# Kernel optimization log

Measured on AMD Instinct MI355X. Metric: run time of the kernel, lower is better.

Reference implementation:

```python
import jax, jax.numpy as jnp
import numpy as np

B, LQ, LC, LN, D, H = 4, 1024, 1024, 1024, 1024, 16
HD = D // H
LS_INIT = 1e-4
RES_MAX = 10.0
EPS = 1e-5


def layernorm(x, g, b):
    mu = jnp.mean(x, axis=-1, keepdims=True)
    var = jnp.var(x, axis=-1, keepdims=True)
    return (x - mu) * jax.lax.rsqrt(var + EPS) * g + b


def setup_inputs() -> dict:
    key = jax.random.key(0)
    ks = jax.random.split(key, 12)
    s = 0.02
    return {
        "tight_tokens": jax.random.normal(ks[0], (B, LQ, D), jnp.float32),
        "context_tokens": jax.random.normal(ks[1], (B, LC, D), jnp.float32),
        "neighborhood_tokens": jax.random.normal(ks[2], (B, LN, D), jnp.float32),
        "ln_q_g": jnp.ones((D,), jnp.float32), "ln_q_b": jnp.zeros((D,), jnp.float32),
        "ln_kv_g": jnp.ones((D,), jnp.float32), "ln_kv_b": jnp.zeros((D,), jnp.float32),
        "in_proj_w": jax.random.normal(ks[3], (3 * D, D), jnp.float32) * s,
        "in_proj_b": jnp.zeros((3 * D,), jnp.float32),
        "out_proj_w": jax.random.normal(ks[4], (D, D), jnp.float32) * s,
        "out_proj_b": jnp.zeros((D,), jnp.float32),
        "cross_gamma": jnp.full((D,), LS_INIT, jnp.float32),
        "ln_f_g": jnp.ones((D,), jnp.float32), "ln_f_b": jnp.zeros((D,), jnp.float32),
        "w1": jax.random.normal(ks[5], (4 * D, D), jnp.float32) * s,
        "b1": jnp.zeros((4 * D,), jnp.float32),
        "w2": jax.random.normal(ks[6], (D, 4 * D), jnp.float32) * s,
        "b2": jnp.zeros((D,), jnp.float32),
        "ffn_gamma": jnp.full((D,), LS_INIT, jnp.float32),
    }


def reference(tight_tokens, context_tokens, neighborhood_tokens,
              ln_q_g, ln_q_b, ln_kv_g, ln_kv_b,
              in_proj_w, in_proj_b, out_proj_w, out_proj_b, cross_gamma,
              ln_f_g, ln_f_b, w1, b1, w2, b2, ffn_gamma):
    kv = jnp.concatenate([context_tokens, neighborhood_tokens], axis=1)  # [B, LKV, D]
    q_in = layernorm(tight_tokens, ln_q_g, ln_q_b)
    kv_in = layernorm(kv, ln_kv_g, ln_kv_b)

    wq, wk, wv = jnp.split(in_proj_w, 3, axis=0)
    bq, bk, bv = jnp.split(in_proj_b, 3, axis=0)
    q = (q_in @ wq.T + bq).reshape(B, LQ, H, HD)
    k = (kv_in @ wk.T + bk).reshape(B, -1, H, HD)
    v = (kv_in @ wv.T + bv).reshape(B, -1, H, HD)

    scores = jnp.einsum('bqhd,bkhd->bhqk', q, k) / jnp.sqrt(jnp.float32(HD))
    attn = jax.nn.softmax(scores, axis=-1)  # [B, H, LQ, LKV]
    ctx = jnp.einsum('bhqk,bkhd->bqhd', attn, v).reshape(B, LQ, D)
    attn_out = ctx @ out_proj_w.T + out_proj_b

    cg = jnp.clip(cross_gamma, -RES_MAX, RES_MAX)
    x = tight_tokens + attn_out * cg

    h = layernorm(x, ln_f_g, ln_f_b)
    h = jax.nn.gelu(h @ w1.T + b1, approximate=False) @ w2.T + b2
    fg = jnp.clip(ffn_gamma, -RES_MAX, RES_MAX)
    x = x + h * fg

    return x, attn.mean(axis=1)
```

## Files before the change

### kernel.cpp

```cpp
#include <hip/hip_runtime.h>
#include <math.h>

typedef unsigned short u16;
typedef __attribute__((ext_vector_type(8))) short bf16x8;
typedef __attribute__((ext_vector_type(4))) float f32x4;

#define MFMA16(a,b,c) __builtin_amdgcn_mfma_f32_16x16x32_bf16(a,b,c,0,0,0)

__device__ __forceinline__ u16 f2bf(float f){
  union { float f; unsigned int u; } x; x.f = f;
  unsigned int r = x.u + 0x7fffu + ((x.u >> 16) & 1u);
  return (u16)(r >> 16);
}

__device__ __forceinline__ void gload16(const void* g, void* lds){
  __builtin_amdgcn_global_load_lds(
    (const __attribute__((address_space(1))) unsigned int*)g,
    (__attribute__((address_space(3))) unsigned int*)lds, 16, 0, 0);
}

__global__ __launch_bounds__(256) void cvt_weights(
    const float* __restrict__ wqkv, const float* __restrict__ wo,
    const float* __restrict__ w1, const float* __restrict__ w2,
    u16* __restrict__ o0, u16* __restrict__ o1,
    u16* __restrict__ o2, u16* __restrict__ o3)
{
  int idx = blockIdx.x * 256 + threadIdx.x;
  const float* src; u16* dst;
  if (idx < 786432)                    { src = wqkv; dst = o0; }
  else if ((idx -= 786432) < 262144)   { src = wo;   dst = o1; }
  else if ((idx -= 262144) < 1048576)  { src = w1;   dst = o2; }
  else { idx -= 1048576;                 src = w2;   dst = o3; }
  float4 v = ((const float4*)src)[idx];
  short4 o;
  o.x = (short)f2bf(v.x); o.y = (short)f2bf(v.y);
  o.z = (short)f2bf(v.z); o.w = (short)f2bf(v.w);
  ((short4*)dst)[idx] = o;
}

template<int MODE>
__global__ __launch_bounds__(256) void ln_kernel(
    const float* __restrict__ s0, const float* __restrict__ s1,
    const float* __restrict__ g, const float* __restrict__ be,
    u16* __restrict__ out)
{
  int row = blockIdx.x, t = threadIdx.x;
  const float* src;
  if (MODE == 1) {
    int b = row >> 11, p = row & 2047;
    src = (p < 1024) ? s0 + ((long)(b*1024 + p))*1024
                     : s1 + ((long)(b*1024 + p - 1024))*1024;
  } else {
    src = s0 + (long)row * 1024;
  }
  float4 v = ((const float4*)src)[t];
  float s  = v.x + v.y + v.z + v.w;
  float ss = v.x*v.x + v.y*v.y + v.z*v.z + v.w*v.w;
  #pragma unroll
  for (int m = 1; m < 64; m <<= 1) { s += __shfl_xor(s, m); ss += __shfl_xor(ss, m); }
  __shared__ float red[8];
  int l = t & 63, w = t >> 6;
  if (l == 0) { red[w*2] = s; red[w*2+1] = ss; }
  __syncthreads();
  s  = red[0] + red[2] + red[4] + red[6];
  ss = red[1] + red[3] + red[5] + red[7];
  float mean = s * (1.0f/1024.0f);
  float var  = ss * (1.0f/1024.0f) - mean*mean;
  float rstd = rsqrtf(var + 1e-5f);
  float4 gv = ((const float4*)g)[t];
  float4 bv = ((const float4*)be)[t];
  short4 o;
  o.x = (short)f2bf((v.x-mean)*rstd*gv.x + bv.x);
  o.y = (short)f2bf((v.y-mean)*rstd*gv.y + bv.y);
  o.z = (short)f2bf((v.z-mean)*rstd*gv.z + bv.z);
  o.w = (short)f2bf((v.w-mean)*rstd*gv.w + bv.w);
  *(short4*)(out + (long)row*1024 + t*4) = o;
}

template<int EPI, int BM>
__global__ __launch_bounds__(256,2) void gemm_bt(
    const u16* __restrict__ A, const u16* __restrict__ Bt,
    int M, int N, int K,
    const float* __restrict__ bias,
    const float* __restrict__ gamma,
    const float* __restrict__ resid,
    float* __restrict__ outf,
    u16* __restrict__ outb0, u16* __restrict__ outb1)
{
  constexpr int MI = BM / 32;
  __shared__ __align__(16) u16 at[2][BM*64];
  __shared__ __align__(16) u16 bt[2][128*64];
  int nwg = gridDim.x;
  int bidx = (blockIdx.x & 7) * (nwg >> 3) + (blockIdx.x >> 3);
  int nb = N >> 7;
  int tm = bidx / nb, tn = bidx % nb;
  int m0 = tm * BM, n0 = tn << 7;
  int t = threadIdx.x, l = t & 63, w = t >> 6;
  int wr = (w >> 1) * (BM/2), wc = (w & 1) * 64;
  int fr = l & 15, fq = l >> 4;
  f32x4 acc[MI][4] = {};
  int rr = t >> 3;
  int cb = (t & 7) << 4;
  const char* Ab = (const char*)A;
  const char* Bp = (const char*)Bt;
  long ld = (long)K * 2;

#define G_STAGE(s, kt) do {                                                        \
    _Pragma("unroll")                                                              \
    for (int c = 0; c < MI; c++) {                                                 \
      int row = c*32 + rr;                                                         \
      gload16(Ab + (long)(m0 + row)*ld + (long)(kt)*2 + (cb ^ ((row & 7) << 4)),   \
              (char*)at[s] + c*4096 + w*1024);                                     \
    }                                                                              \
    _Pragma("unroll")                                                              \
    for (int c = 0; c < 4; c++) {                                                  \
      int row = c*32 + rr;                                                         \
      gload16(Bp + (long)(n0 + row)*ld + (long)(kt)*2 + (cb ^ ((row & 7) << 4)),   \
              (char*)bt[s] + c*4096 + w*1024);                                     \
    }                                                                              \
  } while (0)

  G_STAGE(0, 0);
  __syncthreads();
  int cur = 0;
  for (int kt = 0; kt < K; kt += 64) {
    if (kt + 64 < K) G_STAGE(cur ^ 1, kt + 64);
    #pragma unroll
    for (int ka = 0; ka < 2; ka++) {
      bf16x8 af[MI], bfv[4];
      #pragma unroll
      for (int i = 0; i < MI; i++) {
        int ra = wr + i*16 + fr;
        af[i] = *(const bf16x8*)((const char*)at[cur] + ra*128 + ((ka*64 + fq*16) ^ ((ra & 7) << 4)));
      }
      #pragma unroll
      for (int j = 0; j < 4; j++) {
        int rb = wc + j*16 + fr;
        bfv[j] = *(const bf16x8*)((const char*)bt[cur] + rb*128 + ((ka*64 + fq*16) ^ ((rb & 7) << 4)));
      }
      #pragma unroll
      for (int i = 0; i < MI; i++)
        #pragma unroll
        for (int j = 0; j < 4; j++)
          acc[i][j] = MFMA16(af[i], bfv[j], acc[i][j]);
    }
    __syncthreads();
    cur ^= 1;
  }
#undef G_STAGE
  #pragma unroll
  for (int i = 0; i < MI; i++) {
    #pragma unroll
    for (int j = 0; j < 4; j++) {
      #pragma unroll
      for (int r = 0; r < 4; r++) {
        int row = m0 + wr + i*16 + fq*4 + r;
        int col = n0 + wc + j*16 + fr;
        float v = acc[i][j][r];
        if constexpr (EPI == 0) {
          float qv = (v + bias[col]) * 0.18033688011112042f;
          int b = row >> 10, lq = row & 1023, h = col >> 6, hd = col & 63;
          outb0[(((long)(b*16 + h)) << 16) + (lq << 6) + hd] = f2bf(qv);
        } else if constexpr (EPI == 1) {
          float u = v + bias[col];
          int b = row >> 11, p = row & 2047;
          if (col < 1024) {
            int h = col >> 6, hd = col & 63;
            outb0[(((long)((b*16 + h)*2048 + p)) << 6) + hd] = f2bf(u);
          } else {
            int c2 = col - 1024, h = c2 >> 6, hd = c2 & 63;
            outb1[(((long)((b*16 + h)*64 + hd)) << 11) + p] = f2bf(u);
          }
        } else if constexpr (EPI == 2) {
          float gs = gamma[col]; gs = fminf(fmaxf(gs, -10.f), 10.f);
          long idx = (long)row*1024 + col;
          outf[idx] = resid[idx] + (v + bias[col]) * gs;
        } else if constexpr (EPI == 3) {
          float u = v + bias[col];
          float ge = 0.5f * u * (1.0f + erff(u * 0.70710678118654752f));
          outb0[(long)row*4096 + col] = f2bf(ge);
        } else {
          float gs = gamma[col]; gs = fminf(fmaxf(gs, -10.f), 10.f);
          long idx = (long)row*1024 + col;
          outf[idx] = resid[idx] + (v + bias[col]) * gs;
        }
      }
    }
  }
}

__global__ __launch_bounds__(256, 4) void flash_fwd(
    const u16* __restrict__ q, const u16* __restrict__ k,
    const u16* __restrict__ vt, u16* __restrict__ ctx,
    float* __restrict__ ilout)
{
  __shared__ __align__(16) u16 ks[2][64*64];
  __shared__ __align__(16) u16 vs[2][64*64];
  __shared__ __align__(16) char ps[4*2048];
  int nwg = gridDim.x;
  int bid = (blockIdx.x & 7) * (nwg >> 3) + (blockIdx.x >> 3);
  int qt = bid & 15, h = (bid >> 4) & 15, b = bid >> 8;
  int q0 = qt << 6;
  int t = threadIdx.x, l = t & 63, w = t >> 6;
  int fr = l & 15, fq = l >> 4;
  const char* qb = (const char*)(q  + (((long)(b*16 + h)) << 16));
  const char* kb = (const char*)(k  + (((long)(b*16 + h)) << 17));
  const char* vb = (const char*)(vt + (((long)(b*16 + h)) << 17));
  char* psw = ps + w*2048;
  int rr = t >> 3;
  int sc = (t & 7) << 4;

  #pragma unroll
  for (int c = 0; c < 2; c++) {
    int row = c*32 + rr;
    gload16(kb + (long)row*128 + (sc ^ ((row & 7) << 4)), (char*)ks[0] + c*4096 + w*1024);
    gload16(vb + (long)row*4096 + (sc ^ ((row & 7) << 4)), (char*)vs[0] + c*4096 + w*1024);
  }
  {
    int qr = l >> 3;
    #pragma unroll
    for (int c = 0; c < 2; c++) {
      int row = c*8 + qr;
      gload16(qb + (long)(q0 + w*16 + row)*128 + (sc ^ ((row & 7) << 4)), psw + c*1024);
    }
  }
  asm volatile("s_waitcnt vmcnt(0)" ::: "memory");
  bf16x8 qf0 = *(const bf16x8*)(psw + fr*128 + ((fq*16) ^ ((fr & 7) << 4)));
  bf16x8 qf1 = *(const bf16x8*)(psw + fr*128 + ((64 + fq*16) ^ ((fr & 7) << 4)));
  asm volatile("s_waitcnt lgkmcnt(0)" ::: "memory");
  __builtin_amdgcn_s_barrier();
  asm volatile("" ::: "memory");

  f32x4 cacc[4] = {};
  f32x4 lrun = {0.f, 0.f, 0.f, 0.f};
  int cur = 0;
  for (int kt = 0; kt < 2048; kt += 64) {
    int notlast = (kt + 64 < 2048);
    if (notlast) {
      #pragma unroll
      for (int c = 0; c < 2; c++) {
        int row = c*32 + rr;
        gload16(vb + (long)row*4096 + (long)(kt + 64)*2 + (sc ^ ((row & 7) << 4)),
                (char*)vs[cur ^ 1] + c*4096 + w*1024);
        gload16(kb + (long)(kt + 64 + row)*128 + (sc ^ ((row & 7) << 4)),
                (char*)ks[cur ^ 1] + c*4096 + w*1024);
      }
    }
    __builtin_amdgcn_sched_barrier(0);
    const char* ksb = (const char*)ks[cur];
    f32x4 sf[4];
    __builtin_amdgcn_s_setprio(1);
    #pragma unroll
    for (int cf = 0; cf < 4; cf++) {
      int row = cf*16 + fr;
      bf16x8 kf0 = *(const bf16x8*)(ksb + row*128 + ((fq*16) ^ ((row & 7) << 4)));
      bf16x8 kf1 = *(const bf16x8*)(ksb + row*128 + ((64 + fq*16) ^ ((row & 7) << 4)));
      f32x4 a = {};
      a = MFMA16(qf0, kf0, a);
      sf[cf] = MFMA16(qf1, kf1, a);
    }
    __builtin_amdgcn_s_setprio(0);
    #pragma unroll
    for (int cf = 0; cf < 4; cf++)
      #pragma unroll
      for (int r = 0; r < 4; r++) {
        float pv = exp2f(sf[cf][r]);
        lrun[r] += pv;
        union { float f; unsigned int u; } pu; pu.f = pv;
        int prow = fq*4 + r;
        *(u16*)(psw + prow*128 + (((cf*16 + fr) << 1) ^ ((prow & 7) << 4))) = (u16)(pu.u >> 16);
      }
    bf16x8 pa0 = *(const bf16x8*)(psw + fr*128 + ((fq*16) ^ ((fr & 7) << 4)));
    bf16x8 pa1 = *(const bf16x8*)(psw + fr*128 + ((64 + fq*16) ^ ((fr & 7) << 4)));
    __builtin_amdgcn_s_setprio(1);
    #pragma unroll
    for (int cfd = 0; cfd < 4; cfd++) {
      int hd = cfd*16 + fr;
      bf16x8 vf0 = *(const bf16x8*)((const char*)vs[cur] + hd*128 + ((fq*16) ^ ((hd & 7) << 4)));
      bf16x8 vf1 = *(const bf16x8*)((const char*)vs[cur] + hd*128 + ((64 + fq*16) ^ ((hd & 7) << 4)));
      cacc[cfd] = MFMA16(pa0, vf0, cacc[cfd]);
      cacc[cfd] = MFMA16(pa1, vf1, cacc[cfd]);
    }
    __builtin_amdgcn_s_setprio(0);
    if (notlast) {
      asm volatile("s_waitcnt vmcnt(0)" ::: "memory");
      __builtin_amdgcn_s_barrier();
      asm volatile("" ::: "memory");
    }
    cur ^= 1;
  }
  float il4[4];
  #pragma unroll
  for (int r = 0; r < 4; r++) {
    float s = lrun[r];
    #pragma unroll
    for (int msk = 1; msk < 16; msk <<= 1) s += __shfl_xor(s, msk, 16);
    il4[r] = 1.0f / s;
  }
  #pragma unroll
  for (int cf = 0; cf < 4; cf++)
    #pragma unroll
    for (int r = 0; r < 4; r++) {
      int row = q0 + w*16 + fq*4 + r;
      int col = h*64 + cf*16 + fr;
      ctx[(long)(b*1024 + row)*1024 + col] = f2bf(cacc[cf][r] * il4[r]);
    }
  if (fr == 0) {
    #pragma unroll
    for (int r = 0; r < 4; r++) {
      int row = q0 + w*16 + fq*4 + r;
      long idx = (((long)(b*16 + h)) << 10) + row;
      ilout[idx] = il4[r];
    }
  }
}

__global__ __launch_bounds__(256,2) void attn_mean(
    const u16* __restrict__ q, const u16* __restrict__ k,
    const float* __restrict__ il,
    float* __restrict__ out)
{
  __shared__ __align__(16) u16 qs[2][128*64];
  __shared__ __align__(16) u16 ks[2][128*64];
  __shared__ __align__(16) float ml[2][128];
  int nwg = gridDim.x;
  int bid = (blockIdx.x & 7) * (nwg >> 3) + (blockIdx.x >> 3);
  int kt = bid & 15, qt = (bid >> 4) & 7, b = bid >> 7;
  int q0 = qt << 7, k0 = kt << 7;
  int t = threadIdx.x, l = t & 63, w = t >> 6;
  int wr = (w >> 1) << 6, wc = (w & 1) << 6;
  int fr = l & 15, fq = l >> 4;
  int rr = t >> 3, cbb = (t & 7) << 4;
  const long bh = (long)b * 16;

#define AM_STAGE(hh, s) do {                                                        \
    const char* qb_ = (const char*)(q + ((bh + (hh)) << 16)) + (long)q0*128;        \
    const char* kb_ = (const char*)(k + ((bh + (hh)) << 17)) + (long)k0*128;        \
    _Pragma("unroll")                                                               \
    for (int c = 0; c < 4; c++) {                                                   \
      int row = c*32 + rr;                                                          \
      int sw = cbb ^ ((row & 7) << 4);                                              \
      gload16(qb_ + (long)row*128 + sw, (char*)qs[s] + c*4096 + w*1024);            \
      gload16(kb_ + (long)row*128 + sw, (char*)ks[s] + c*4096 + w*1024);            \
    }                                                                               \
    if (w == 0 && l < 32) {                                                         \
      gload16((const char*)(il + ((bh + (hh)) << 10) + q0) + l*16, (char*)ml[s]);   \
    }                                                                               \
  } while (0)

  AM_STAGE(0, 0);
  asm volatile("s_waitcnt vmcnt(0)" ::: "memory");
  __builtin_amdgcn_s_barrier();
  asm volatile("" ::: "memory");

  f32x4 macc[4][4] = {};
  for (int h = 0; h < 16; h++) {
    int cur = h & 1;
    if (h < 15) AM_STAGE(h + 1, cur ^ 1);
    const char* qsb = (const char*)qs[cur];
    const char* ksb = (const char*)ks[cur];
    const float* mlb = ml[cur];
    f32x4 ir4[4];
    #pragma unroll
    for (int i = 0; i < 4; i++)
      ir4[i] = *(const f32x4*)(mlb + wr + i*16 + fq*4);
    bf16x8 af[4][2], bf[4][2];
    #pragma unroll
    for (int i = 0; i < 4; i++) {
      int ra = wr + i*16 + fr;
      int rb = wc + i*16 + fr;
      af[i][0] = *(const bf16x8*)(qsb + ra*128 + ((fq*16) ^ ((ra & 7) << 4)));
      af[i][1] = *(const bf16x8*)(qsb + ra*128 + ((64 + fq*16) ^ ((ra & 7) << 4)));
      bf[i][0] = *(const bf16x8*)(ksb + rb*128 + ((fq*16) ^ ((rb & 7) << 4)));
      bf[i][1] = *(const bf16x8*)(ksb + rb*128 + ((64 + fq*16) ^ ((rb & 7) << 4)));
    }
    #pragma unroll
    for (int j = 0; j < 4; j++) {
      f32x4 sf[4];
      __builtin_amdgcn_s_setprio(1);
      #pragma unroll
      for (int i = 0; i < 4; i++) {
        f32x4 a = MFMA16(af[i][0], bf[j][0], {});
        sf[i] = MFMA16(af[i][1], bf[j][1], a);
      }
      __builtin_amdgcn_s_setprio(0);
      #pragma unroll
      for (int i = 0; i < 4; i++)
        #pragma unroll
        for (int r = 0; r < 4; r++)
          macc[i][j][r] += exp2f(sf[i][r]) * ir4[i][r];
    }
    asm volatile("s_waitcnt vmcnt(0)" ::: "memory");
    __builtin_amdgcn_s_barrier();
    asm volatile("" ::: "memory");
  }
#undef AM_STAGE
  #pragma unroll
  for (int i = 0; i < 4; i++)
    #pragma unroll
    for (int j = 0; j < 4; j++)
      #pragma unroll
      for (int r = 0; r < 4; r++) {
        int row = q0 + wr + i*16 + fq*4 + r;
        int col = k0 + wc + j*16 + fr;
        out[((long)(b*1024 + row) << 11) + col] = macc[i][j][r] * 0.0625f;
      }
}

extern "C" void kernel_launch(void* const* d_in, const int* in_sizes, int n_in,
                              void* d_out, int out_size, void* d_ws, size_t ws_size,
                              hipStream_t stream)
{
  (void)in_sizes; (void)n_in; (void)out_size; (void)ws_size;
  const float* tight = (const float*)d_in[0];
  const float* ctxt  = (const float*)d_in[1];
  const float* nbh   = (const float*)d_in[2];
  const float* lnqg  = (const float*)d_in[3];
  const float* lnqb  = (const float*)d_in[4];
  const float* lnkg  = (const float*)d_in[5];
  const float* lnkb  = (const float*)d_in[6];
  const float* wqkv  = (const float*)d_in[7];
  const float* bqkv  = (const float*)d_in[8];
  const float* wo    = (const float*)d_in[9];
  const float* bo    = (const float*)d_in[10];
  const float* cg    = (const float*)d_in[11];
  const float* lnfg  = (const float*)d_in[12];
  const float* lnfb  = (const float*)d_in[13];
  const float* w1    = (const float*)d_in[14];
  const float* b1    = (const float*)d_in[15];
  const float* w2    = (const float*)d_in[16];
  const float* b2    = (const float*)d_in[17];
  const float* fg    = (const float*)d_in[18];

  char* p = (char*)d_ws;
  u16* wqkv_bf = (u16*)p; p += 3072L*1024*2;
  u16* wo_bf   = (u16*)p; p += 1024L*1024*2;
  u16* w1_bf   = (u16*)p; p += 4096L*1024*2;
  u16* w2_bf   = (u16*)p; p += 1024L*4096*2;
  u16* qin_bf  = (u16*)p; p += 4096L*1024*2;
  u16* kvin_bf = (u16*)p; p += 8192L*1024*2;
  u16* q_bf    = (u16*)p; p += 4L*16*1024*64*2;
  u16* k_bf    = (u16*)p; p += 4L*16*2048*64*2;
  u16* vt_bf   = (u16*)p; p += 4L*16*64*2048*2;
  u16* ctx_bf  = (u16*)p; p += 4096L*1024*2;
  float* il_f  = (float*)p; p += 4L*16*1024*4;
  float* x_f   = (float*)p; p += 4096L*1024*4;
  u16* hln_bf  = (u16*)p; p += 4096L*1024*2;
  u16* gelu_bf = (u16*)p; p += 4096L*4096*2;

  float* x_out    = (float*)d_out;
  float* mean_out = x_out + 4194304;

  cvt_weights<<<12288, 256, 0, stream>>>(wqkv, wo, w1, w2, wqkv_bf, wo_bf, w1_bf, w2_bf);
  ln_kernel<0><<<4096, 256, 0, stream>>>(tight, nullptr, lnqg, lnqb, qin_bf);
  ln_kernel<1><<<8192, 256, 0, stream>>>(ctxt, nbh, lnkg, lnkb, kvin_bf);
  gemm_bt<0,64><<<512, 256, 0, stream>>>(qin_bf, wqkv_bf, 4096, 1024, 1024,
                                      bqkv, nullptr, nullptr, nullptr, q_bf, nullptr);
  gemm_bt<1,128><<<1024, 256, 0, stream>>>(kvin_bf, wqkv_bf + 1024L*1024, 8192, 2048, 1024,
                                       bqkv + 1024, nullptr, nullptr, nullptr, k_bf, vt_bf);
  flash_fwd<<<1024, 256, 0, stream>>>(q_bf, k_bf, vt_bf, ctx_bf, il_f);
  attn_mean<<<512, 256, 0, stream>>>(q_bf, k_bf, il_f, mean_out);
  gemm_bt<2,64><<<512, 256, 0, stream>>>(ctx_bf, wo_bf, 4096, 1024, 1024,
                                      bo, cg, tight, x_f, nullptr, nullptr);
  ln_kernel<0><<<4096, 256, 0, stream>>>(x_f, nullptr, lnfg, lnfb, hln_bf);
  gemm_bt<3,128><<<1024, 256, 0, stream>>>(hln_bf, w1_bf, 4096, 4096, 1024,
                                       b1, nullptr, nullptr, nullptr, gelu_bf, nullptr);
  gemm_bt<4,64><<<512, 256, 0, stream>>>(gelu_bf, w2_bf, 4096, 1024, 4096,
                                      b2, fg, x_f, x_out, nullptr, nullptr);
}
```

Baseline: 374.1 us.

## Double query rows per wave in flash attention to reuse K/V tiles

Each workgroup now handles 128 query rows instead of 64, with every wave computing two 16-row fragments that share the same K and V fragments loaded from LDS. This halves the number of K/V tile loads from global memory and the LDS fragment reads per MFMA, and the grid shrinks from 1024 to 512 workgroups. The cost is more registers and a larger P buffer in LDS, with occupancy lowered to 3 waves-per-SIMD bound, and fewer workgroups to spread across compute units.

New measurement: 371.7 us. About the same (-0.6%).

```diff
diff --git a/kernel.cpp b/kernel.cpp
--- a/kernel.cpp
+++ b/kernel.cpp
@@ -189,24 +189,24 @@
   }
 }
 
-__global__ __launch_bounds__(256, 4) void flash_fwd(
+__global__ __launch_bounds__(256, 3) void flash_fwd(
     const u16* __restrict__ q, const u16* __restrict__ k,
     const u16* __restrict__ vt, u16* __restrict__ ctx,
     float* __restrict__ ilout)
 {
   __shared__ __align__(16) u16 ks[2][64*64];
   __shared__ __align__(16) u16 vs[2][64*64];
-  __shared__ __align__(16) char ps[4*2048];
+  __shared__ __align__(16) char ps[4*4096];
   int nwg = gridDim.x;
   int bid = (blockIdx.x & 7) * (nwg >> 3) + (blockIdx.x >> 3);
-  int qt = bid & 15, h = (bid >> 4) & 15, b = bid >> 8;
-  int q0 = qt << 6;
+  int qt = bid & 7, h = (bid >> 3) & 15, b = bid >> 7;
+  int q0 = qt << 7;
   int t = threadIdx.x, l = t & 63, w = t >> 6;
   int fr = l & 15, fq = l >> 4;
   const char* qb = (const char*)(q  + (((long)(b*16 + h)) << 16));
   const char* kb = (const char*)(k  + (((long)(b*16 + h)) << 17));
   const char* vb = (const char*)(vt + (((long)(b*16 + h)) << 17));
-  char* psw = ps + w*2048;
+  char* psw = ps + w*4096;
   int rr = t >> 3;
   int sc = (t & 7) << 4;
 
@@ -219,20 +219,25 @@
   {
     int qr = l >> 3;
     #pragma unroll
-    for (int c = 0; c < 2; c++) {
+    for (int c = 0; c < 4; c++) {
       int row = c*8 + qr;
-      gload16(qb + (long)(q0 + w*16 + row)*128 + (sc ^ ((row & 7) << 4)), psw + c*1024);
+      gload16(qb + (long)(q0 + w*32 + row)*128 + (sc ^ ((row & 7) << 4)), psw + c*1024);
     }
   }
   asm volatile("s_waitcnt vmcnt(0)" ::: "memory");
-  bf16x8 qf0 = *(const bf16x8*)(psw + fr*128 + ((fq*16) ^ ((fr & 7) << 4)));
-  bf16x8 qf1 = *(const bf16x8*)(psw + fr*128 + ((64 + fq*16) ^ ((fr & 7) << 4)));
+  bf16x8 qf[2][2];
+  #pragma unroll
+  for (int rf = 0; rf < 2; rf++) {
+    int row = rf*16 + fr;
+    qf[rf][0] = *(const bf16x8*)(psw + row*128 + ((fq*16) ^ ((row & 7) << 4)));
+    qf[rf][1] = *(const bf16x8*)(psw + row*128 + ((64 + fq*16) ^ ((row & 7) << 4)));
+  }
   asm volatile("s_waitcnt lgkmcnt(0)" ::: "memory");
   __builtin_amdgcn_s_barrier();
   asm volatile("" ::: "memory");
 
-  f32x4 cacc[4] = {};
-  f32x4 lrun = {0.f, 0.f, 0.f, 0.f};
+  f32x4 cacc[2][4] = {};
+  f32x4 lrun[2] = {{0.f,0.f,0.f,0.f},{0.f,0.f,0.f,0.f}};
   int cur = 0;
   for (int kt = 0; kt < 2048; kt += 64) {
     int notlast = (kt + 64 < 2048);
@@ -248,38 +253,51 @@
     }
     __builtin_amdgcn_sched_barrier(0);
     const char* ksb = (const char*)ks[cur];
-    f32x4 sf[4];
+    f32x4 sf[2][4];
     __builtin_amdgcn_s_setprio(1);
     #pragma unroll
     for (int cf = 0; cf < 4; cf++) {
       int row = cf*16 + fr;
       bf16x8 kf0 = *(const bf16x8*)(ksb + row*128 + ((fq*16) ^ ((row & 7) << 4)));
       bf16x8 kf1 = *(const bf16x8*)(ksb + row*128 + ((64 + fq*16) ^ ((row & 7) << 4)));
-      f32x4 a = {};
-      a = MFMA16(qf0, kf0, a);
-      sf[cf] = MFMA16(qf1, kf1, a);
+      #pragma unroll
+      for (int rf = 0; rf < 2; rf++) {
+        f32x4 a = {};
+        a = MFMA16(qf[rf][0], kf0, a);
+        sf[rf][cf] = MFMA16(qf[rf][1], kf1, a);
+      }
     }
     __builtin_amdgcn_s_setprio(0);
     #pragma unroll
-    for (int cf = 0; cf < 4; cf++)
-      #pragma unroll
-      for (int r = 0; r < 4; r++) {
-        float pv = exp2f(sf[cf][r]);
-        lrun[r] += pv;
-        union { float f; unsigned int u; } pu; pu.f = pv;
-        int prow = fq*4 + r;
-        *(u16*)(psw + prow*128 + (((cf*16 + fr) << 1) ^ ((prow & 7) << 4))) = (u16)(pu.u >> 16);
-      }
-    bf16x8 pa0 = *(const bf16x8*)(psw + fr*128 + ((fq*16) ^ ((fr & 7) << 4)));
-    bf16x8 pa1 = *(const bf16x8*)(psw + fr*128 + ((64 + fq*16) ^ ((fr & 7) << 4)));
+    for (int rf = 0; rf < 2; rf++)
+      #pragma unroll
+      for (int cf = 0; cf < 4; cf++)
+        #pragma unroll
+        for (int r = 0; r < 4; r++) {
+          float pv = exp2f(sf[rf][cf][r]);
+          lrun[rf][r] += pv;
+          union { float f; unsigned int u; } pu; pu.f = pv;
+          int prow = rf*16 + fq*4 + r;
+          *(u16*)(psw + prow*128 + (((cf*16 + fr) << 1) ^ ((prow & 7) << 4))) = (u16)(pu.u >> 16);
+        }
+    bf16x8 pa[2][2];
+    #pragma unroll
+    for (int rf = 0; rf < 2; rf++) {
+      int row = rf*16 + fr;
+      pa[rf][0] = *(const bf16x8*)(psw + row*128 + ((fq*16) ^ ((row & 7) << 4)));
+      pa[rf][1] = *(const bf16x8*)(psw + row*128 + ((64 + fq*16) ^ ((row & 7) << 4)));
+    }
     __builtin_amdgcn_s_setprio(1);
     #pragma unroll
     for (int cfd = 0; cfd < 4; cfd++) {
       int hd = cfd*16 + fr;
       bf16x8 vf0 = *(const bf16x8*)((const char*)vs[cur] + hd*128 + ((fq*16) ^ ((hd & 7) << 4)));
       bf16x8 vf1 = *(const bf16x8*)((const char*)vs[cur] + hd*128 + ((64 + fq*16) ^ ((hd & 7) << 4)));
-      cacc[cfd] = MFMA16(pa0, vf0, cacc[cfd]);
-      cacc[cfd] = MFMA16(pa1, vf1, cacc[cfd]);
+      #pragma unroll
+      for (int rf = 0; rf < 2; rf++) {
+        cacc[rf][cfd] = MFMA16(pa[rf][0], vf0, cacc[rf][cfd]);
+        cacc[rf][cfd] = MFMA16(pa[rf][1], vf1, cacc[rf][cfd]);
+      }
     }
     __builtin_amdgcn_s_setprio(0);
     if (notlast) {
@@ -289,28 +307,31 @@
     }
     cur ^= 1;
   }
-  float il4[4];
-  #pragma unroll
-  for (int r = 0; r < 4; r++) {
-    float s = lrun[r];
-    #pragma unroll
-    for (int msk = 1; msk < 16; msk <<= 1) s += __shfl_xor(s, msk, 16);
-    il4[r] = 1.0f / s;
-  }
-  #pragma unroll
-  for (int cf = 0; cf < 4; cf++)
+  #pragma unroll
+  for (int rf = 0; rf < 2; rf++) {
+    float il4[4];
     #pragma unroll
     for (int r = 0; r < 4; r++) {
-      int row = q0 + w*16 + fq*4 + r;
-      int col = h*64 + cf*16 + fr;
-      ctx[(long)(b*1024 + row)*1024 + col] = f2bf(cacc[cf][r] * il4[r]);
-    }
-  if (fr == 0) {
-    #pragma unroll
-    for (int r = 0; r < 4; r++) {
-      int row = q0 + w*16 + fq*4 + r;
-      long idx = (((long)(b*16 + h)) << 10) + row;
-      ilout[idx] = il4[r];
+      float s = lrun[rf][r];
+      #pragma unroll
+      for (int msk = 1; msk < 16; msk <<= 1) s += __shfl_xor(s, msk, 16);
+      il4[r] = 1.0f / s;
+    }
+    #pragma unroll
+    for (int cf = 0; cf < 4; cf++)
+      #pragma unroll
+      for (int r = 0; r < 4; r++) {
+        int row = q0 + w*32 + rf*16 + fq*4 + r;
+        int col = h*64 + cf*16 + fr;
+        ctx[(long)(b*1024 + row)*1024 + col] = f2bf(cacc[rf][cf][r] * il4[r]);
+      }
+    if (fr == 0) {
+      #pragma unroll
+      for (int r = 0; r < 4; r++) {
+        int row = q0 + w*32 + rf*16 + fq*4 + r;
+        long idx = (((long)(b*16 + h)) << 10) + row;
+        ilout[idx] = il4[r];
+      }
     }
   }
 }
@@ -458,7 +479,7 @@
                                       bqkv, nullptr, nullptr, nullptr, q_bf, nullptr);
   gemm_bt<1,128><<<1024, 256, 0, stream>>>(kvin_bf, wqkv_bf + 1024L*1024, 8192, 2048, 1024,
                                        bqkv + 1024, nullptr, nullptr, nullptr, k_bf, vt_bf);
-  flash_fwd<<<1024, 256, 0, stream>>>(q_bf, k_bf, vt_bf, ctx_bf, il_f);
+  flash_fwd<<<512, 256, 0, stream>>>(q_bf, k_bf, vt_bf, ctx_bf, il_f);
   attn_mean<<<512, 256, 0, stream>>>(q_bf, k_bf, il_f, mean_out);
   gemm_bt<2,64><<<512, 256, 0, stream>>>(ctx_bf, wo_bf, 4096, 1024, 1024,
                                       bo, cg, tight, x_f, nullptr, nullptr);
```
